# Optimization experiments

Hardware: AMD Instinct MI355X
Metric: run time of the kernel (lower is better)

## Reference

```python
import jax, jax.numpy as jnp
import numpy as np

N_NODES = 50000
N_EDGES = 800000
D_IN = 128
D_OUT = 128


def setup_inputs() -> dict:
    key = jax.random.key(0)
    k1, k2, k3, k4, k5, k6 = jax.random.split(key, 6)
    x = jax.random.normal(k1, (N_NODES, D_IN), dtype=jnp.float32)
    edge_src = jax.random.randint(k2, (N_EDGES,), 0, N_NODES, dtype=jnp.int32)
    edge_dst = jax.random.randint(k3, (N_EDGES,), 0, N_NODES, dtype=jnp.int32)
    edge_val = jax.random.uniform(k4, (N_EDGES,), dtype=jnp.float32)
    stdv = 1.0 / np.sqrt(D_OUT)
    weight = jax.random.uniform(k5, (D_IN, D_OUT), dtype=jnp.float32, minval=-stdv, maxval=stdv)
    bias = jax.random.uniform(k6, (D_OUT,), dtype=jnp.float32, minval=-stdv, maxval=stdv)
    return {"x": x, "edge_src": edge_src, "edge_dst": edge_dst,
            "edge_val": edge_val, "weight": weight, "bias": bias}


def reference(x, edge_src, edge_dst, edge_val, weight, bias):
    # support = input @ W   ([N, D_out])
    support = jnp.matmul(x, weight)
    # SpMM: out[i] = sum_{e: dst[e]==i} val[e] * support[src[e]]
    gathered = support[edge_src] * edge_val[:, None]          # [E, D_out]
    out = jax.ops.segment_sum(gathered, edge_dst, num_segments=N_NODES)
    return out + bias
```

## Files before the change

### kernel.cpp

```cpp
#include <hip/hip_runtime.h>
#include <hip/hip_fp16.h>

#define D 128
#define ELLW 32
#define OVF_CAP 65536
#define LDK 136

typedef short short8 __attribute__((ext_vector_type(8)));
typedef float floatx4 __attribute__((ext_vector_type(4)));

__device__ __forceinline__ unsigned short f2bf(float f) {
    unsigned u = __float_as_uint(f);
    u += 0x7fff + ((u >> 16) & 1);
    return (unsigned short)(u >> 16);
}

__global__ __launch_bounds__(256) void gc_fused(const float* __restrict__ x,
                                                const float* __restrict__ w,
                                                unsigned short* __restrict__ support,
                                                const int* __restrict__ esrc,
                                                const int* __restrict__ edst,
                                                const float* __restrict__ eval,
                                                int* __restrict__ cnt,
                                                unsigned* __restrict__ ell,
                                                int* __restrict__ ovf_cnt,
                                                uint4* __restrict__ ovf,
                                                int n_nodes, int n_edges) {
    __shared__ unsigned short xl[64 * LDK];
    __shared__ unsigned short wl[D * LDK];

    const int tid = threadIdx.x;

    if (blockIdx.x & 1) {
        int t = (blockIdx.x >> 1) * 256 + tid;
        int e0 = t * 4;
        if (e0 >= n_edges) return;

        auto put = [&](int d, int s, float v, int slot) {
            if (slot < ELLW) {
                unsigned entry = ((unsigned)s << 16) |
                                 (unsigned)__half_as_ushort(__float2half(v));
                __builtin_nontemporal_store(entry, &ell[(size_t)d * ELLW + slot]);
            } else {
                int p = atomicAdd(ovf_cnt, 1);
                if (p < OVF_CAP) ovf[p] = make_uint4((unsigned)s, (unsigned)d,
                                                     __float_as_uint(v), 0u);
            }
        };

        if (e0 + 3 < n_edges) {
            int4   s4 = ((const int4*)esrc)[t];
            int4   d4 = ((const int4*)edst)[t];
            float4 v4 = ((const float4*)eval)[t];
            int sl0 = atomicAdd(&cnt[d4.x], 1);
            int sl1 = atomicAdd(&cnt[d4.y], 1);
            int sl2 = atomicAdd(&cnt[d4.z], 1);
            int sl3 = atomicAdd(&cnt[d4.w], 1);
            put(d4.x, s4.x, v4.x, sl0);
            put(d4.y, s4.y, v4.y, sl1);
            put(d4.z, s4.z, v4.z, sl2);
            put(d4.w, s4.w, v4.w, sl3);
        } else {
            for (int e = e0; e < n_edges; ++e) {
                int d = edst[e], s = esrc[e];
                float v = eval[e];
                int slot = atomicAdd(&cnt[d], 1);
                put(d, s, v, slot);
            }
        }
        return;
    }

    const int row0 = (blockIdx.x >> 1) * 64;

    const float4* w4g = (const float4*)w;
    for (int i = tid; i < D * 32; i += 256) {
        int k = i >> 5, n4 = i & 31;
        float4 v = w4g[i];
        wl[(n4 * 4 + 0) * LDK + k] = f2bf(v.x);
        wl[(n4 * 4 + 1) * LDK + k] = f2bf(v.y);
        wl[(n4 * 4 + 2) * LDK + k] = f2bf(v.z);
        wl[(n4 * 4 + 3) * LDK + k] = f2bf(v.w);
    }
    const float4* x4 = (const float4*)x;
    for (int i = tid; i < 64 * 32; i += 256) {
        int r = i >> 5, k4 = i & 31;
        int row = row0 + r;
        ushort4 p = {0, 0, 0, 0};
        if (row < n_nodes) {
            float4 v = x4[(size_t)row * 32 + k4];
            p.x = f2bf(v.x); p.y = f2bf(v.y); p.z = f2bf(v.z); p.w = f2bf(v.w);
        }
        *(ushort4*)(&xl[r * LDK + k4 * 4]) = p;
    }
    __syncthreads();

    const int wv = tid >> 6;
    const int l  = tid & 63;
    const int lr = l & 15;
    const int lk = (l >> 4) * 8;

    floatx4 acc[8];
#pragma unroll
    for (int ct = 0; ct < 8; ++ct) acc[ct] = (floatx4){0.f, 0.f, 0.f, 0.f};

#pragma unroll
    for (int ks = 0; ks < 4; ++ks) {
        short8 a = *(const short8*)(&xl[(wv * 16 + lr) * LDK + ks * 32 + lk]);
#pragma unroll
        for (int ct = 0; ct < 8; ++ct) {
            short8 b = *(const short8*)(&wl[(ct * 16 + lr) * LDK + ks * 32 + lk]);
            acc[ct] = __builtin_amdgcn_mfma_f32_16x16x32_bf16(a, b, acc[ct], 0, 0, 0);
        }
    }

    const int rbase = row0 + wv * 16 + (l >> 4) * 4;
#pragma unroll
    for (int r = 0; r < 4; ++r) {
        int row = rbase + r;
        if (row < n_nodes) {
#pragma unroll
            for (int ct = 0; ct < 8; ++ct)
                support[(size_t)row * D + ct * 16 + lr] = f2bf(acc[ct][r]);
        }
    }
}

__global__ __launch_bounds__(256) void gc_gather_ell(const unsigned* __restrict__ support,
                                                     const int* __restrict__ cnt,
                                                     const unsigned* __restrict__ ell,
                                                     const float* __restrict__ bias,
                                                     const int* __restrict__ ovf_cnt,
                                                     const uint4* __restrict__ ovf,
                                                     float* __restrict__ out, int n) {
    int node = blockIdx.x * 4 + (threadIdx.x >> 6);
    int lane = threadIdx.x & 63;
    if (node >= n) return;

    int deg = cnt[node];
    deg = (deg < ELLW) ? deg : ELLW;
    deg = __builtin_amdgcn_readfirstlane(deg);

    unsigned mine = ell[(size_t)node * ELLW + (lane & 31)];
    float2 acc = ((const float2*)bias)[lane];

    unsigned e0 = 0, e1 = 0, e2 = 0, e3 = 0, e4 = 0, e5 = 0, e6 = 0, e7 = 0;
    unsigned g0 = 0, g1 = 0, g2 = 0, g3 = 0, g4 = 0, g5 = 0, g6 = 0, g7 = 0;

#define PRE(J, E, G)                                                          \
    if (J < deg) {                                                            \
        E = __shfl(mine, J);                                                  \
        int sr = __builtin_amdgcn_readfirstlane((int)(E >> 16));              \
        G = support[(size_t)sr * 64 + lane];                                  \
    }
    PRE(0, e0, g0) PRE(1, e1, g1) PRE(2, e2, g2) PRE(3, e3, g3)
    PRE(4, e4, g4) PRE(5, e5, g5) PRE(6, e6, g6) PRE(7, e7, g7)
#undef PRE

#define STEP(E, G, NX)                                                        \
    {                                                                         \
        float v = __half2float(__ushort_as_half((unsigned short)(E & 0xffffu))); \
        acc.x = fmaf(v, __uint_as_float(G << 16), acc.x);                     \
        acc.y = fmaf(v, __uint_as_float(G & 0xffff0000u), acc.y);             \
        if ((NX) < deg) {                                                     \
            E = __shfl(mine, (NX) & 31);                                      \
            int sr = __builtin_amdgcn_readfirstlane((int)(E >> 16));          \
            G = support[(size_t)sr * 64 + lane];                              \
        } else {                                                              \
            E = 0;                                                            \
        }                                                                     \
    }
    for (int s = 0; s < deg; s += 8) {
        STEP(e0, g0, s + 8)  STEP(e1, g1, s + 9)
        STEP(e2, g2, s + 10) STEP(e3, g3, s + 11)
        STEP(e4, g4, s + 12) STEP(e5, g5, s + 13)
        STEP(e6, g6, s + 14) STEP(e7, g7, s + 15)
    }
#undef STEP

    int novf = *ovf_cnt;
    novf = (novf < OVF_CAP) ? novf : OVF_CAP;
    novf = __builtin_amdgcn_readfirstlane(novf);
    for (int i = 0; i < novf; ++i) {
        uint4 e = ovf[i];
        if ((int)e.y == node) {
            float v = __uint_as_float(e.z);
            unsigned g = support[(size_t)e.x * 64 + lane];
            acc.x = fmaf(v, __uint_as_float(g << 16), acc.x);
            acc.y = fmaf(v, __uint_as_float(g & 0xffff0000u), acc.y);
        }
    }

    ((float2*)out)[(size_t)node * 64 + lane] = acc;
}

extern "C" void kernel_launch(void* const* d_in, const int* in_sizes, int n_in,
                              void* d_out, int out_size, void* d_ws, size_t ws_size,
                              hipStream_t stream) {
    const float* x        = (const float*)d_in[0];
    const int*   edge_src = (const int*)d_in[1];
    const int*   edge_dst = (const int*)d_in[2];
    const float* edge_val = (const float*)d_in[3];
    const float* weight   = (const float*)d_in[4];
    const float* bias     = (const float*)d_in[5];
    float*       out      = (float*)d_out;

    const int n_nodes = in_sizes[0] / D;
    const int n_edges = in_sizes[1];

    size_t off = 0;
    auto take = [&](size_t bytes) {
        size_t p = off;
        off = (off + bytes + 255) & ~(size_t)255;
        return p;
    };
    char* ws = (char*)d_ws;
    size_t o_ovfcnt  = take(256);
    size_t o_cnt     = take((size_t)n_nodes * 4);
    size_t o_ell     = take((size_t)n_nodes * ELLW * 4);
    size_t o_ovf     = take((size_t)OVF_CAP * 16);
    size_t o_support = take((size_t)n_nodes * D * 2);
    (void)ws_size;

    int* ovf_cnt        = (int*)(ws + o_ovfcnt);
    int* cnt            = (int*)(ws + o_cnt);
    unsigned* ell       = (unsigned*)(ws + o_ell);
    uint4* ovf          = (uint4*)(ws + o_ovf);
    unsigned short* sup = (unsigned short*)(ws + o_support);

    hipMemsetAsync(ws + o_ovfcnt, 0, o_ell - o_ovfcnt, stream);

    int gemm_blocks = (n_nodes + 63) / 64;
    int fill_blocks = ((n_edges + 3) / 4 + 255) / 256;
    int total = 2 * ((gemm_blocks > fill_blocks) ? gemm_blocks : fill_blocks);
    gc_fused<<<total, 256, 0, stream>>>(x, weight, sup,
                                        edge_src, edge_dst, edge_val,
                                        cnt, ell, ovf_cnt, ovf,
                                        n_nodes, n_edges);

    gc_gather_ell<<<(n_nodes + 3) / 4, 256, 0, stream>>>(
        (const unsigned*)sup, cnt, ell, bias, ovf_cnt, ovf, out, n_nodes);
}
```

Baseline: 166.2 us.

## Split each wave into four edge groups with 16-byte bf16 gathers

```diff
diff --git a/kernel.cpp b/kernel.cpp
--- a/kernel.cpp
+++ b/kernel.cpp
@@ -14,6 +14,9 @@
     u += 0x7fff + ((u >> 16) & 1);
     return (unsigned short)(u >> 16);
 }
+
+__device__ __forceinline__ float bf_lo(unsigned g) { return __uint_as_float(g << 16); }
+__device__ __forceinline__ float bf_hi(unsigned g) { return __uint_as_float(g & 0xffff0000u); }
 
 __global__ __launch_bounds__(256) void gc_fused(const float* __restrict__ x,
                                                 const float* __restrict__ w,
@@ -73,14 +76,14 @@
 
     const int row0 = (blockIdx.x >> 1) * 64;
 
-    const float4* w4g = (const float4*)w;
     for (int i = tid; i < D * 32; i += 256) {
-        int k = i >> 5, n4 = i & 31;
-        float4 v = w4g[i];
-        wl[(n4 * 4 + 0) * LDK + k] = f2bf(v.x);
-        wl[(n4 * 4 + 1) * LDK + k] = f2bf(v.y);
-        wl[(n4 * 4 + 2) * LDK + k] = f2bf(v.z);
-        wl[(n4 * 4 + 3) * LDK + k] = f2bf(v.w);
+        int n = i & 127, k0 = (i >> 7) << 2;
+        ushort4 p;
+        p.x = f2bf(w[(k0 + 0) * D + n]);
+        p.y = f2bf(w[(k0 + 1) * D + n]);
+        p.z = f2bf(w[(k0 + 2) * D + n]);
+        p.w = f2bf(w[(k0 + 3) * D + n]);
+        *(ushort4*)(&wl[n * LDK + k0]) = p;
     }
     const float4* x4 = (const float4*)x;
     for (int i = tid; i < 64 * 32; i += 256) {
@@ -126,13 +129,13 @@
     }
 }
 
-__global__ __launch_bounds__(256) void gc_gather_ell(const unsigned* __restrict__ support,
+__global__ __launch_bounds__(256) void gc_gather_ell(const uint4* __restrict__ sup4,
                                                      const int* __restrict__ cnt,
                                                      const unsigned* __restrict__ ell,
                                                      const float* __restrict__ bias,
                                                      const int* __restrict__ ovf_cnt,
                                                      const uint4* __restrict__ ovf,
-                                                     float* __restrict__ out, int n) {
+                                                     float4* __restrict__ out4, int n) {
     int node = blockIdx.x * 4 + (threadIdx.x >> 6);
     int lane = threadIdx.x & 63;
     if (node >= n) return;
@@ -142,40 +145,38 @@
     deg = __builtin_amdgcn_readfirstlane(deg);
 
     unsigned mine = ell[(size_t)node * ELLW + (lane & 31)];
-    float2 acc = ((const float2*)bias)[lane];
-
-    unsigned e0 = 0, e1 = 0, e2 = 0, e3 = 0, e4 = 0, e5 = 0, e6 = 0, e7 = 0;
-    unsigned g0 = 0, g1 = 0, g2 = 0, g3 = 0, g4 = 0, g5 = 0, g6 = 0, g7 = 0;
+    const int q  = lane >> 4;
+    const int sl = lane & 15;
+
+    float a0 = 0.f, a1 = 0.f, a2 = 0.f, a3 = 0.f,
+          a4 = 0.f, a5 = 0.f, a6 = 0.f, a7 = 0.f;
+
+    const uint4 z4 = make_uint4(0u, 0u, 0u, 0u);
+    unsigned E0, E1, E2, E3, E4, E5, E6, E7;
+    uint4    G0, G1, G2, G3, G4, G5, G6, G7;
 
 #define PRE(J, E, G)                                                          \
-    if (J < deg) {                                                            \
-        E = __shfl(mine, J);                                                  \
-        int sr = __builtin_amdgcn_readfirstlane((int)(E >> 16));              \
-        G = support[(size_t)sr * 64 + lane];                                  \
-    }
-    PRE(0, e0, g0) PRE(1, e1, g1) PRE(2, e2, g2) PRE(3, e3, g3)
-    PRE(4, e4, g4) PRE(5, e5, g5) PRE(6, e6, g6) PRE(7, e7, g7)
+    {                                                                         \
+        int s_ = (J) * 4 + q;                                      \
+        E = __shfl(mine, s_);                    \
+        if (s_ < deg) {                                                       \
+            G = sup4[(size_t)(E >> 16) * 16 + sl];                            \
+        } else { E = 0u; G = z4; }                                            \
+    }
+    PRE(0, E0, G0) PRE(1, E1, G1) PRE(2, E2, G2) PRE(3, E3, G3)
+    PRE(4, E4, G4) PRE(5, E5, G5) PRE(6, E6, G6) PRE(7, E7, G7)
 #undef PRE
 
-#define STEP(E, G, NX)                                                        \
+#define STEP(E, G)                                                            \
     {                                                                         \
         float v = __half2float(__ushort_as_half((unsigned short)(E & 0xffffu))); \
-        acc.x = fmaf(v, __uint_as_float(G << 16), acc.x);                     \
-        acc.y = fmaf(v, __uint_as_float(G & 0xffff0000u), acc.y);             \
-        if ((NX) < deg) {                                                     \
-            E = __shfl(mine, (NX) & 31);                                      \
-            int sr = __builtin_amdgcn_readfirstlane((int)(E >> 16));          \
-            G = support[(size_t)sr * 64 + lane];                              \
-        } else {                                                              \
-            E = 0;                                                            \
-        }                                                                     \
-    }
-    for (int s = 0; s < deg; s += 8) {
-        STEP(e0, g0, s + 8)  STEP(e1, g1, s + 9)
-        STEP(e2, g2, s + 10) STEP(e3, g3, s + 11)
-        STEP(e4, g4, s + 12) STEP(e5, g5, s + 13)
-        STEP(e6, g6, s + 14) STEP(e7, g7, s + 15)
-    }
+        a0 = fmaf(v, bf_lo(G.x), a0); a1 = fmaf(v, bf_hi(G.x), a1);           \
+        a2 = fmaf(v, bf_lo(G.y), a2); a3 = fmaf(v, bf_hi(G.y), a3);           \
+        a4 = fmaf(v, bf_lo(G.z), a4); a5 = fmaf(v, bf_hi(G.z), a5);           \
+        a6 = fmaf(v, bf_lo(G.w), a6); a7 = fmaf(v, bf_hi(G.w), a7);           \
+    }
+    STEP(E0, G0) STEP(E1, G1) STEP(E2, G2) STEP(E3, G3)
+    STEP(E4, G4) STEP(E5, G5) STEP(E6, G6) STEP(E7, G7)
 #undef STEP
 
     int novf = *ovf_cnt;
@@ -183,15 +184,29 @@
     novf = __builtin_amdgcn_readfirstlane(novf);
     for (int i = 0; i < novf; ++i) {
         uint4 e = ovf[i];
-        if ((int)e.y == node) {
+        if ((int)e.y == node && q == 0) {
             float v = __uint_as_float(e.z);
-            unsigned g = support[(size_t)e.x * 64 + lane];
-            acc.x = fmaf(v, __uint_as_float(g << 16), acc.x);
-            acc.y = fmaf(v, __uint_as_float(g & 0xffff0000u), acc.y);
-        }
-    }
-
-    ((float2*)out)[(size_t)node * 64 + lane] = acc;
+            uint4 g = sup4[(size_t)e.x * 16 + sl];
+            a0 = fmaf(v, bf_lo(g.x), a0); a1 = fmaf(v, bf_hi(g.x), a1);
+            a2 = fmaf(v, bf_lo(g.y), a2); a3 = fmaf(v, bf_hi(g.y), a3);
+            a4 = fmaf(v, bf_lo(g.z), a4); a5 = fmaf(v, bf_hi(g.z), a5);
+            a6 = fmaf(v, bf_lo(g.w), a6); a7 = fmaf(v, bf_hi(g.w), a7);
+        }
+    }
+
+#define RED(A) A += __shfl_xor(A, 16); A += __shfl_xor(A, 32);
+    RED(a0) RED(a1) RED(a2) RED(a3) RED(a4) RED(a5) RED(a6) RED(a7)
+#undef RED
+
+    if (q < 2) {
+        const float4* b4 = (const float4*)bias;
+        float4 r;
+        if (q == 0) { r.x = a0; r.y = a1; r.z = a2; r.w = a3; }
+        else        { r.x = a4; r.y = a5; r.z = a6; r.w = a7; }
+        float4 bb = b4[sl * 2 + q];
+        r.x += bb.x; r.y += bb.y; r.z += bb.z; r.w += bb.w;
+        out4[(size_t)node * 32 + sl * 2 + q] = r;
+    }
 }
 
 extern "C" void kernel_launch(void* const* d_in, const int* in_sizes, int n_in,
@@ -203,7 +218,6 @@
     const float* edge_val = (const float*)d_in[3];
     const float* weight   = (const float*)d_in[4];
     const float* bias     = (const float*)d_in[5];
-    float*       out      = (float*)d_out;
 
     const int n_nodes = in_sizes[0] / D;
     const int n_edges = in_sizes[1];
@@ -239,5 +253,6 @@
                                         n_nodes, n_edges);
 
     gc_gather_ell<<<(n_nodes + 3) / 4, 256, 0, stream>>>(
-        (const unsigned*)sup, cnt, ell, bias, ovf_cnt, ovf, out, n_nodes);
-}
+        (const uint4*)sup, cnt, ell, bias, ovf_cnt, ovf,
+        (float4*)d_out, n_nodes);
+}
```

Result: faster. 152.9 us (-8.0%).
